# Optimization experiments

Hardware: AMD Instinct MI355X
Metric: run time of the kernel (lower is better)

Reference implementation:

```python
import jax, jax.numpy as jnp
import numpy as np

B, N, D, H = 4, 2048, 768, 12
HD = D // H
SCALE = HD ** -0.5


def setup_inputs() -> dict:
    key = jax.random.key(0)
    k1, k2, k3 = jax.random.split(key, 3)
    x = jax.random.normal(k1, (B, N, D), dtype=jnp.float32)
    w_qkv = jax.random.normal(k2, (D, 3 * D), dtype=jnp.float32) * (D ** -0.5)
    w_proj = jax.random.normal(k3, (D, D), dtype=jnp.float32) * (D ** -0.5)
    b_proj = jnp.zeros((D,), dtype=jnp.float32)
    return {"x": x, "w_qkv": w_qkv, "w_proj": w_proj, "b_proj": b_proj}


def reference(x, w_qkv, w_proj, b_proj):
    b, n, d = x.shape
    qkv = x @ w_qkv                      # [b, n, 3d]
    q, k, v = jnp.split(qkv, 3, axis=-1)
    # [b, n, d] -> [b, h, n, hd]
    split_heads = lambda t: t.reshape(b, n, H, HD).transpose(0, 2, 1, 3)
    q, k, v = split_heads(q), split_heads(k), split_heads(v)
    dots = jnp.einsum('bhqd,bhkd->bhqk', q, k) * SCALE   # [b, h, n, n]
    attn = jax.nn.softmax(dots, axis=-1)
    q_attn = attn[:, :, 0, :]            # attention row of query token 0: [b, h, n]
    # dropout p=0 (eval) -> identity
    out = jnp.einsum('bhqk,bhkd->bhqd', attn, v)          # [b, h, n, hd]
    out = out.transpose(0, 2, 1, 3).reshape(b, n, d)      # [b, n, d]
    return out @ w_proj + b_proj, q_attn
```

## Files before the change

### kernel.cpp

```cpp
#include <hip/hip_runtime.h>


typedef unsigned short u16;
typedef __attribute__((ext_vector_type(8))) short bf8;
typedef __attribute__((ext_vector_type(4))) short bf4;
typedef __attribute__((ext_vector_type(4))) int i4;
typedef __attribute__((ext_vector_type(4))) float f4;

#define MFMA16(a, b, c) __builtin_amdgcn_mfma_f32_16x16x32_bf16((a), (b), (c), 0, 0, 0)

#if __has_builtin(__builtin_amdgcn_exp2f)
#define EXP2(x) __builtin_amdgcn_exp2f(x)
#else
#define EXP2(x) __expf((x) * 0.6931471805599453f)
#endif

__device__ __forceinline__ float b2f(u16 h) {
  union { unsigned u; float f; } v; v.u = ((unsigned)h) << 16; return v.f;
}
__device__ __forceinline__ u16 f2b(float f) {
  union { float f; unsigned u; } v; v.f = f;
  unsigned r = v.u + 0x7fffu + ((v.u >> 16) & 1u);
  return (u16)(r >> 16);
}
__device__ __forceinline__ unsigned pack2(float a, float b) {
#if __has_builtin(__builtin_amdgcn_perm)
  return __builtin_amdgcn_perm(__builtin_bit_cast(unsigned, b),
                               __builtin_bit_cast(unsigned, a), 0x07060302u);
#else
  return (__builtin_bit_cast(unsigned, b) & 0xFFFF0000u) |
         (__builtin_bit_cast(unsigned, a) >> 16);
#endif
}
__device__ __forceinline__ void gload16(const u16* g, u16* l) {
  __builtin_amdgcn_global_load_lds(
      (const __attribute__((address_space(1))) void*)g,
      (__attribute__((address_space(3))) void*)l, 16, 0, 0);
}
__device__ __forceinline__ int detect_f32(const u16* x) {
  unsigned v = x[2 * (threadIdx.x & 63)];
  unsigned e = (v >> 7) & 0xFF;
  return __ballot(e >= 0x8E) != 0ull;
}

__global__ __launch_bounds__(256) void prep(
    const void* __restrict__ x, u16* __restrict__ xbf,
    const void* __restrict__ wqkv, u16* __restrict__ wqkvT,
    const void* __restrict__ wproj, u16* __restrict__ wprojT) {
  const int z = blockIdx.z;
  if (z == 2) {
    const int f32 = detect_f32((const u16*)x);
    const int lin = blockIdx.y * 72 + blockIdx.x;
    if (f32) {
      const float2* in = (const float2*)x;
      unsigned* out = (unsigned*)xbf;
      for (int i = lin * 256 + threadIdx.x; i < 3145728; i += 442368) {
        float2 v = in[i];
        out[i] = (unsigned)f2b(v.x) | ((unsigned)f2b(v.y) << 16);
      }
    } else {
      const unsigned* in = (const unsigned*)x;
      unsigned* out = (unsigned*)xbf;
      for (int i = lin * 256 + threadIdx.x; i < 3145728; i += 442368)
        out[i] = in[i];
    }
    return;
  }
  if (z == 1 && blockIdx.x >= 24) return;
  const void* in = z ? wproj : wqkv;
  u16* out = z ? wprojT : wqkvT;
  const int R = 768, C = z ? 768 : 2304;
  __shared__ u16 tile[32][33];
  const int f32 = detect_f32((const u16*)x);
  const int bx = blockIdx.x * 32, by = blockIdx.y * 32;
  const int tx = threadIdx.x & 31, ty = threadIdx.x >> 5;
#pragma unroll
  for (int i = 0; i < 4; i++) {
    size_t idx = (size_t)(by + ty + i * 8) * C + bx + tx;
    tile[ty + i * 8][tx] = f32 ? f2b(((const float*)in)[idx]) : ((const u16*)in)[idx];
  }
  __syncthreads();
#pragma unroll
  for (int i = 0; i < 4; i++)
    out[(size_t)(bx + ty + i * 8) * R + by + tx] = tile[tx][ty + i * 8];
}

__global__ __launch_bounds__(512, 2) void gemm_qkv8(
    const u16* __restrict__ A, const u16* __restrict__ Bt,
    u16* __restrict__ Cq, u16* __restrict__ Vt) {
  __shared__ alignas(16) u16 L[2][34816];
  const int t = threadIdx.x;
  const int lane = t & 63, wave = t >> 6;
  const int wr = wave >> 1, wc = wave & 1;
  const int quad = lane >> 4, l16 = lane & 15;
  const int bm = blockIdx.y * 256, bn = blockIdx.x * 288;
  const int dcol = ((lane & 3) ^ ((lane >> 3) & 3)) * 8;
  const int swzU = (quad ^ ((l16 >> 1) & 3)) * 8;
  const int drow = lane >> 2;
  f4 acc[4][9] = {};

#define STAGE_ALL(kt, buf)                                                   \
  for (int c = wave; c < 68; c += 8) {                                       \
    const int isB = c >= 32;                                                 \
    const int cb = isB ? c - 32 : c;                                         \
    const int kq_ = isB ? (cb >= 18 ? 1 : 0) : (cb >> 4);                    \
    const int r16 = isB ? (cb - kq_ * 18) : (cb & 15);                       \
    const u16* src = (isB ? Bt : A) +                                        \
        (size_t)((isB ? bn : bm) + r16 * 16 + drow) * 768 +                  \
        (kt) * 64 + kq_ * 32 + dcol;                                         \
    u16* dst = &L[buf][(isB ? 16384 + kq_ * 9216 : kq_ * 8192) + r16 * 512]; \
    gload16(src, dst);                                                       \
  }

  STAGE_ALL(0, 0);
  asm volatile("s_waitcnt vmcnt(0)" ::: "memory");
  __builtin_amdgcn_sched_barrier(0);
  __builtin_amdgcn_s_barrier();
  __builtin_amdgcn_sched_barrier(0);

  for (int j = 0; j < 12; j++) {
    const int buf = j & 1;
    if (j + 1 < 12) STAGE_ALL(j + 1, buf ^ 1);
    const u16* Lb = &L[buf][0];
    bf8 af[4][2];
#pragma unroll
    for (int m = 0; m < 4; m++)
#pragma unroll
      for (int kq = 0; kq < 2; kq++)
        af[m][kq] = *(const bf8*)&Lb[kq * 8192 +
                                     (wr * 64 + m * 16 + l16) * 32 + swzU];
#pragma unroll
    for (int p = 0; p < 3; p++) {
      bf8 bfr[3][2];
#pragma unroll
      for (int nn = 0; nn < 3; nn++)
#pragma unroll
        for (int kq = 0; kq < 2; kq++)
          bfr[nn][kq] = *(const bf8*)&Lb[16384 + kq * 9216 +
              (wc * 144 + (p * 3 + nn) * 16 + l16) * 32 + swzU];
      __builtin_amdgcn_s_setprio(1);
#pragma unroll
      for (int nn = 0; nn < 3; nn++)
#pragma unroll
        for (int m = 0; m < 4; m++) {
          acc[m][p * 3 + nn] = MFMA16(af[m][0], bfr[nn][0], acc[m][p * 3 + nn]);
          acc[m][p * 3 + nn] = MFMA16(af[m][1], bfr[nn][1], acc[m][p * 3 + nn]);
        }
      __builtin_amdgcn_s_setprio(0);
    }
    if (j + 1 < 12) {
      asm volatile("s_waitcnt vmcnt(0)" ::: "memory");
      __builtin_amdgcn_sched_barrier(0);
      __builtin_amdgcn_s_barrier();
      __builtin_amdgcn_sched_barrier(0);
    }
  }
#undef STAGE_ALL

  const int b_ = bm >> 11;
#pragma unroll
  for (int m = 0; m < 4; m++) {
    const int row0 = bm + wr * 64 + m * 16 + quad * 4;
    const int n0 = row0 & 2047;
    const int n2 = (n0 & ~31) | (((n0 >> 2) & 3) << 3) | (((n0 >> 4) & 1) << 2);
#pragma unroll
    for (int ni = 0; ni < 9; ni++) {
      const int col = bn + wc * 144 + ni * 16 + l16;
      if (col >= 1536) {
        const int colv = col - 1536, h = colv >> 6, d = colv & 63;
        bf4 pk = {(short)f2b(acc[m][ni][0]), (short)f2b(acc[m][ni][1]),
                  (short)f2b(acc[m][ni][2]), (short)f2b(acc[m][ni][3])};
        *(bf4*)&Vt[(size_t)((b_ * 12 + h) * 64 + d) * 2048 + n2] = pk;
      } else {
#pragma unroll
        for (int r = 0; r < 4; r++)
          Cq[(size_t)(row0 + r) * 2304 + col] = f2b(acc[m][ni][r]);
      }
    }
  }
}

template <int BIAS, int QATTN>
__global__ __launch_bounds__(256, 4) void gemm_bt(
    const u16* __restrict__ A, const u16* __restrict__ Bt,
    const void* __restrict__ bias, void* __restrict__ C,
    int M, int Ncols, int K, const u16* __restrict__ xdet,
    u16* __restrict__ Vt, const float* __restrict__ qe,
    const float* __restrict__ lout) {
  if (QATTN && blockIdx.x == 6) {
    const int f32o = detect_f32(xdet);
    const int base = blockIdx.y * 1536;
    for (int j = threadIdx.x; j < 1536; j += 256) {
      int idx = base + j;
      float v = qe[idx] * (1.f / lout[idx >> 11]);
      size_t oidx = (size_t)6291456 + idx;
      if (f32o) ((float*)C)[oidx] = v; else ((u16*)C)[oidx] = f2b(v);
    }
    return;
  }
  __shared__ alignas(16) u16 Al[2][128 * 32];
  __shared__ alignas(16) u16 Bl[2][128 * 32];
  const int t = threadIdx.x;
  const int lane = t & 63, wave = t >> 6;
  const int wr = wave >> 1, wc = wave & 1;
  const int quad = lane >> 4, l16 = lane & 15;
  const int bm = blockIdx.y * 128, bn = blockIdx.x * 128;
  const int f32o = BIAS ? detect_f32(xdet) : 0;
  const int grow = lane >> 2, gcol = (lane & 3) * 8;
  const int chunk0 = wave * 2, chunk1 = wave * 2 + 1;
  const int arow0 = chunk0 * 16 + grow, arow1 = chunk1 * 16 + grow;
  f4 acc[4][4] = {};
  gload16(A + (size_t)(bm + arow0) * K + gcol, &Al[0][chunk0 * 512]);
  gload16(Bt + (size_t)(bn + arow0) * K + gcol, &Bl[0][chunk0 * 512]);
  gload16(A + (size_t)(bm + arow1) * K + gcol, &Al[0][chunk1 * 512]);
  gload16(Bt + (size_t)(bn + arow1) * K + gcol, &Bl[0][chunk1 * 512]);
  const int NIT = K >> 5;
  for (int i = 0; i < NIT; i++) {
    const int cur = i & 1, nxt = cur ^ 1;
    __syncthreads();
    if (i + 1 < NIT) {
      int k0 = (i + 1) << 5;
      gload16(A + (size_t)(bm + arow0) * K + k0 + gcol, &Al[nxt][chunk0 * 512]);
      gload16(Bt + (size_t)(bn + arow0) * K + k0 + gcol, &Bl[nxt][chunk0 * 512]);
      gload16(A + (size_t)(bm + arow1) * K + k0 + gcol, &Al[nxt][chunk1 * 512]);
      gload16(Bt + (size_t)(bn + arow1) * K + k0 + gcol, &Bl[nxt][chunk1 * 512]);
    }
    bf8 af[4], bfr[4];
#pragma unroll
    for (int mt = 0; mt < 4; mt++)
      af[mt] = *(const bf8*)&Al[cur][(wr * 64 + mt * 16 + l16) * 32 + quad * 8];
#pragma unroll
    for (int nt = 0; nt < 4; nt++)
      bfr[nt] = *(const bf8*)&Bl[cur][(wc * 64 + nt * 16 + l16) * 32 + quad * 8];
#pragma unroll
    for (int mt = 0; mt < 4; mt++)
#pragma unroll
      for (int nt = 0; nt < 4; nt++)
        acc[mt][nt] = MFMA16(af[mt], bfr[nt], acc[mt][nt]);
  }
  if (Vt != nullptr && bn >= 1536) {
    const int b = bm >> 11;
#pragma unroll
    for (int mt = 0; mt < 4; mt++) {
      int n0 = (bm & 2047) + wr * 64 + mt * 16 + quad * 4;
      int n2 = (n0 & ~31) | (((n0 >> 2) & 3) << 3) | (((n0 >> 4) & 1) << 2);
#pragma unroll
      for (int nt = 0; nt < 4; nt++) {
        int colv = bn - 1536 + wc * 64 + nt * 16 + l16;
        int h = colv >> 6, d = colv & 63;
        bf4 pk = {(short)f2b(acc[mt][nt][0]), (short)f2b(acc[mt][nt][1]),
                  (short)f2b(acc[mt][nt][2]), (short)f2b(acc[mt][nt][3])};
        *(bf4*)&Vt[(size_t)((b * 12 + h) * 64 + d) * 2048 + n2] = pk;
      }
    }
    return;
  }
#pragma unroll
  for (int mt = 0; mt < 4; mt++) {
    int row = bm + wr * 64 + mt * 16 + quad * 4;
#pragma unroll
    for (int nt = 0; nt < 4; nt++) {
      int col = bn + wc * 64 + nt * 16 + l16;
      float bv = 0.f;
      if (BIAS)
        bv = f32o ? ((const float*)bias)[col] : b2f(((const u16*)bias)[col]);
#pragma unroll
      for (int r = 0; r < 4; r++) {
        size_t idx = (size_t)(row + r) * Ncols + col;
        float v = acc[mt][nt][r] + bv;
        if (f32o) ((float*)C)[idx] = v; else ((u16*)C)[idx] = f2b(v);
      }
    }
  }
}

__global__ __launch_bounds__(256, 3) void flash_attn(
    const u16* __restrict__ qkv, const u16* __restrict__ Vt,
    u16* __restrict__ O, float* __restrict__ qe, float* __restrict__ lout) {
  __shared__ alignas(16) u16 lds[3][8192];
  const int t = threadIdx.x, lane = t & 63, wave = t >> 6;
  const int quad = lane >> 4, l16 = lane & 15;
  const int id = blockIdx.x;
  const int bh = (id & 7) + 8 * (id >> 7);
  const int qtile = (id >> 3) & 15;
  const int b = bh / 12, h = bh - b * 12;
  const int q0 = qtile * 128 + wave * 32;
  const bool dumpP = (qe != nullptr) && (qtile == 0) && (wave == 0);
  const float SCALE2 = 0.125f * 1.44269504089f;
  const float mM0 = -16.f;
  bf8 qf[2][2];
#pragma unroll
  for (int qt = 0; qt < 2; qt++) {
    const u16* Qr = qkv + (size_t)(b * 2048 + q0 + qt * 16 + l16) * 2304 + h * 64;
    bf8 r0 = *(const bf8*)(Qr + quad * 8);
    bf8 r1 = *(const bf8*)(Qr + 32 + quad * 8);
#pragma unroll
    for (int j = 0; j < 8; j++) {
      qf[qt][0][j] = (short)f2b(b2f((u16)r0[j]) * SCALE2);
      qf[qt][1][j] = (short)f2b(b2f((u16)r1[j]) * SCALE2);
    }
  }
  bf8 ones;
#pragma unroll
  for (int j = 0; j < 8; j++) ones[j] = (short)0x3F80;
  const u16* Kb = qkv + (size_t)(b * 2048) * 2304 + 768 + h * 64;
  const u16* Vb = Vt + (size_t)((b * 12 + h) * 64) * 2048;
  const int drow = wave * 16 + (lane >> 2);
  const int dcol = ((lane & 3) ^ ((lane >> 3) & 3)) * 8;
  const int swz = (quad ^ ((l16 >> 1) & 3)) * 8;
  f4 o[2][4] = {};
  f4 lacc[2] = {};

#define STAGE(tile, buf)                                            \
  {                                                                 \
    int n1_ = (tile) * 64;                                          \
    const u16* Kt_ = Kb + (size_t)(n1_ + drow) * 2304 + dcol;       \
    const u16* Vr_ = Vb + (size_t)drow * 2048 + n1_ + dcol;         \
    u16* base_ = &lds[buf][wave * 512];                             \
    gload16(Kt_, base_);                                            \
    gload16(Kt_ + 32, base_ + 2048);                                \
    gload16(Vr_, base_ + 4096);                                     \
    gload16(Vr_ + 32, base_ + 6144);                                \
  }

  STAGE(0, 0);
  STAGE(1, 1);

  int cur = 0;
  for (int i = 0; i < 32; i++) {
    if (i < 31) {
      asm volatile("s_waitcnt vmcnt(4)" ::: "memory");
    } else {
      asm volatile("s_waitcnt vmcnt(0)" ::: "memory");
    }
    __builtin_amdgcn_s_barrier();
    if (i + 2 < 32) {
      int pre = cur + 2; if (pre >= 3) pre -= 3;
      STAGE(i + 2, pre);
    }
    const u16* K0 = &lds[cur][0];
    const u16* K1 = &lds[cur][2048];
    union { i4 i; bf8 b; } pf[2][2];
#pragma unroll
    for (int kt = 0; kt < 4; kt++) {
      bf8 kf0 = *(const bf8*)&K0[(kt * 16 + l16) * 32 + swz];
      bf8 kf1 = *(const bf8*)&K1[(kt * 16 + l16) * 32 + swz];
#pragma unroll
      for (int qt = 0; qt < 2; qt++) {
        f4 z = {mM0, mM0, mM0, mM0};
        z = MFMA16(kf0, qf[qt][0], z);
        z = MFMA16(kf1, qf[qt][1], z);
        float e0 = EXP2(z[0]);
        float e1 = EXP2(z[1]);
        float e2 = EXP2(z[2]);
        float e3 = EXP2(z[3]);
        if (qt == 0 && dumpP && l16 == 0) {
          f4 ev = {e0, e1, e2, e3};
          *(f4*)&qe[bh * 2048 + i * 64 + kt * 16 + quad * 4] = ev;
        }
        pf[qt][kt >> 1].i[(kt & 1) * 2 + 0] = (int)pack2(e0, e1);
        pf[qt][kt >> 1].i[(kt & 1) * 2 + 1] = (int)pack2(e2, e3);
      }
    }
#pragma unroll
    for (int pair = 0; pair < 2; pair++) {
      const u16* Vp = &lds[cur][4096 + pair * 2048];
      lacc[0] = MFMA16(ones, pf[0][pair].b, lacc[0]);
      lacc[1] = MFMA16(ones, pf[1][pair].b, lacc[1]);
#pragma unroll
      for (int nt = 0; nt < 4; nt++) {
        bf8 vf = *(const bf8*)&Vp[(nt * 16 + l16) * 32 + swz];
        o[0][nt] = MFMA16(vf, pf[0][pair].b, o[0][nt]);
        o[1][nt] = MFMA16(vf, pf[1][pair].b, o[1][nt]);
      }
    }
    cur = (cur == 2) ? 0 : cur + 1;
  }
#undef STAGE
#pragma unroll
  for (int qt = 0; qt < 2; qt++) {
    float l = lacc[qt][0];
    if (qt == 0 && dumpP && lane == 0) lout[bh] = l;
    float inv = 1.f / l;
    size_t row = (size_t)(b * 2048 + q0 + qt * 16 + l16) * 768 + h * 64;
#pragma unroll
    for (int nt = 0; nt < 4; nt++) {
      bf4 pk = {(short)f2b(o[qt][nt][0] * inv), (short)f2b(o[qt][nt][1] * inv),
                (short)f2b(o[qt][nt][2] * inv), (short)f2b(o[qt][nt][3] * inv)};
      *(bf4*)&O[row + nt * 16 + quad * 4] = pk;
    }
  }
}

__global__ __launch_bounds__(256) void qattn_row0(
    const u16* __restrict__ qkv, void* __restrict__ out,
    const u16* __restrict__ xdet) {
  const int bh = blockIdx.x, b = bh / 12, h = bh % 12;
  __shared__ float qs[64];
  __shared__ float sv[2048];
  __shared__ float red[8];
  const int t = threadIdx.x;
  const int f32o = detect_f32(xdet);
  if (t < 64) qs[t] = b2f(qkv[(size_t)(b * 2048) * 2304 + h * 64 + t]);
  __syncthreads();
  float lmax = -1e30f;
  for (int k = t; k < 2048; k += 256) {
    const u16* Kr = qkv + (size_t)(b * 2048 + k) * 2304 + 768 + h * 64;
    float acc = 0.f;
#pragma unroll
    for (int j = 0; j < 8; j++) {
      bf8 kv = *(const bf8*)(Kr + j * 8);
#pragma unroll
      for (int d = 0; d < 8; d++) acc += qs[j * 8 + d] * b2f((u16)kv[d]);
    }
    acc *= 0.125f;
    sv[k] = acc;
    lmax = fmaxf(lmax, acc);
  }
#pragma unroll
  for (int off = 32; off >= 1; off >>= 1) lmax = fmaxf(lmax, __shfl_xor(lmax, off, 64));
  if ((t & 63) == 0) red[t >> 6] = lmax;
  __syncthreads();
  const float bmax = fmaxf(fmaxf(red[0], red[1]), fmaxf(red[2], red[3]));
  float lsum = 0.f;
  for (int k = t; k < 2048; k += 256) {
    float e = __expf(sv[k] - bmax);
    sv[k] = e;
    lsum += e;
  }
#pragma unroll
  for (int off = 32; off >= 1; off >>= 1) lsum += __shfl_xor(lsum, off, 64);
  if ((t & 63) == 0) red[4 + (t >> 6)] = lsum;
  __syncthreads();
  const float inv = 1.f / (red[4] + red[5] + red[6] + red[7]);
  for (int k = t; k < 2048; k += 256) {
    size_t idx = (size_t)6291456 + (size_t)bh * 2048 + k;
    float v = sv[k] * inv;
    if (f32o) ((float*)out)[idx] = v; else ((u16*)out)[idx] = f2b(v);
  }
}

extern "C" void kernel_launch(void* const* d_in, const int* in_sizes, int n_in,
                              void* d_out, int out_size, void* d_ws, size_t ws_size,
                              hipStream_t stream) {
  const void* x_raw      = d_in[0];
  const void* w_qkv_raw  = d_in[1];
  const void* w_proj_raw = d_in[2];
  const void* b_proj_raw = d_in[3];
  const u16* xdet = (const u16*)x_raw;
  char* ws = (char*)d_ws;
  u16* xbf    = (u16*)(ws + 256);
  u16* wqkvT  = (u16*)(ws + 12583168);
  u16* wprojT = (u16*)(ws + 16122112);
  u16* qkv    = (u16*)(ws + 17301760);
  u16* Vt     = (u16*)(ws + 55050496);
  float* qe   = (float*)(ws + 67633408);
  float* lout = (float*)(ws + 68026624);
  u16* attn   = xbf;
  const bool fused = ws_size >= 68026816ull;

  prep<<<dim3(72, 24, 3), 256, 0, stream>>>(
      x_raw, xbf, w_qkv_raw, wqkvT, w_proj_raw, wprojT);
  gemm_qkv8<<<dim3(8, 32), 512, 0, stream>>>(xbf, wqkvT, qkv, Vt);
  flash_attn<<<dim3(768), 256, 0, stream>>>(qkv, Vt, attn,
                                            fused ? qe : nullptr,
                                            fused ? lout : nullptr);
  if (fused) {
    gemm_bt<1, 1><<<dim3(7, 64), 256, 0, stream>>>(
        attn, wprojT, b_proj_raw, d_out, 8192, 768, 768, xdet, nullptr, qe, lout);
  } else {
    gemm_bt<1, 0><<<dim3(6, 64), 256, 0, stream>>>(
        attn, wprojT, b_proj_raw, d_out, 8192, 768, 768, xdet, nullptr, nullptr, nullptr);
    qattn_row0<<<dim3(48), 256, 0, stream>>>(qkv, d_out, xdet);
  }
}
```

Before: 209.4 us.

## Software-pipeline attention loop so QK-exp of one tile overlaps PV of previous

Unrolls the 32-tile key loop into a two-stage software pipeline. The QK^T MFMA and exp2 for tile i now run alongside the PV MFMAs for tile i-1. V fragments are preloaded from LDS into registers after each QK stage, and the probability tiles ping-pong between two register sets. The aim is to hide the exp/pack latency and the dependency between QK and PV so the MFMA pipe stays busy. In exchange it adds about 32 VGPRs for V plus a second probability buffer, which may lower occupancy, and it adds an lgkmcnt(0) wait at each barrier.

```diff
diff --git a/kernel.cpp b/kernel.cpp
--- a/kernel.cpp
+++ b/kernel.cpp
@@ -6,6 +6,7 @@
 typedef __attribute__((ext_vector_type(4))) short bf4;
 typedef __attribute__((ext_vector_type(4))) int i4;
 typedef __attribute__((ext_vector_type(4))) float f4;
+typedef union { i4 iv; bf8 bv; } pfu;
 
 #define MFMA16(a, b, c) __builtin_amdgcn_mfma_f32_16x16x32_bf16((a), (b), (c), 0, 0, 0)
 
@@ -310,6 +311,9 @@
   const int swz = (quad ^ ((l16 >> 1) & 3)) * 8;
   f4 o[2][4] = {};
   f4 lacc[2] = {};
+  pfu pfA[2][2], pfB[2][2];
+  bf8 vf[8];
+  int cur = 0;
 
 #define STAGE(tile, buf)                                            \
   {                                                                 \
@@ -323,60 +327,111 @@
     gload16(Vr_ + 32, base_ + 6144);                                \
   }
 
+#define HEAD(DRAIN, DOSTAGE, i)                                          \
+  {                                                                      \
+    if (DRAIN) { asm volatile("s_waitcnt vmcnt(0) lgkmcnt(0)" ::: "memory"); } \
+    else { asm volatile("s_waitcnt vmcnt(4) lgkmcnt(0)" ::: "memory"); } \
+    __builtin_amdgcn_s_barrier();                                        \
+    if (DOSTAGE) {                                                       \
+      int pre_ = cur + 2; if (pre_ >= 3) pre_ -= 3;                      \
+      STAGE((i) + 2, pre_);                                              \
+    }                                                                    \
+  }
+
+#define QKEXP(i, PFC)                                                    \
+  {                                                                      \
+    const u16* K0_ = &lds[cur][0];                                       \
+    const u16* K1_ = &lds[cur][2048];                                    \
+    _Pragma("unroll")                                                    \
+    for (int kt = 0; kt < 4; kt++) {                                     \
+      bf8 kf0 = *(const bf8*)&K0_[(kt * 16 + l16) * 32 + swz];           \
+      bf8 kf1 = *(const bf8*)&K1_[(kt * 16 + l16) * 32 + swz];           \
+      _Pragma("unroll")                                                  \
+      for (int qt = 0; qt < 2; qt++) {                                   \
+        f4 z = {mM0, mM0, mM0, mM0};                                     \
+        z = MFMA16(kf0, qf[qt][0], z);                                   \
+        z = MFMA16(kf1, qf[qt][1], z);                                   \
+        float e0 = EXP2(z[0]);                                           \
+        float e1 = EXP2(z[1]);                                           \
+        float e2 = EXP2(z[2]);                                           \
+        float e3 = EXP2(z[3]);                                           \
+        if (qt == 0 && dumpP && l16 == 0) {                              \
+          f4 ev = {e0, e1, e2, e3};                                      \
+          *(f4*)&qe[bh * 2048 + (i) * 64 + kt * 16 + quad * 4] = ev;     \
+        }                                                                \
+        PFC[qt][kt >> 1].iv[(kt & 1) * 2 + 0] = (int)pack2(e0, e1);      \
+        PFC[qt][kt >> 1].iv[(kt & 1) * 2 + 1] = (int)pack2(e2, e3);      \
+      }                                                                  \
+    }                                                                    \
+  }
+
+#define PV(PFP)                                                          \
+  {                                                                      \
+    _Pragma("unroll")                                                    \
+    for (int pair = 0; pair < 2; pair++) {                               \
+      lacc[0] = MFMA16(ones, PFP[0][pair].bv, lacc[0]);                  \
+      lacc[1] = MFMA16(ones, PFP[1][pair].bv, lacc[1]);                  \
+      _Pragma("unroll")                                                  \
+      for (int nt = 0; nt < 4; nt++) {                                   \
+        o[0][nt] = MFMA16(vf[nt * 2 + pair], PFP[0][pair].bv, o[0][nt]); \
+        o[1][nt] = MFMA16(vf[nt * 2 + pair], PFP[1][pair].bv, o[1][nt]); \
+      }                                                                  \
+    }                                                                    \
+  }
+
+#define LOADVF                                                           \
+  {                                                                      \
+    _Pragma("unroll")                                                    \
+    for (int pair = 0; pair < 2; pair++) {                               \
+      const u16* Vp_ = &lds[cur][4096 + pair * 2048];                    \
+      _Pragma("unroll")                                                  \
+      for (int nt = 0; nt < 4; nt++)                                     \
+        vf[nt * 2 + pair] = *(const bf8*)&Vp_[(nt * 16 + l16) * 32 + swz]; \
+    }                                                                    \
+  }
+
+#define ADV cur = (cur == 2) ? 0 : cur + 1;
+
   STAGE(0, 0);
   STAGE(1, 1);
-
-  int cur = 0;
-  for (int i = 0; i < 32; i++) {
-    if (i < 31) {
-      asm volatile("s_waitcnt vmcnt(4)" ::: "memory");
-    } else {
-      asm volatile("s_waitcnt vmcnt(0)" ::: "memory");
-    }
-    __builtin_amdgcn_s_barrier();
-    if (i + 2 < 32) {
-      int pre = cur + 2; if (pre >= 3) pre -= 3;
-      STAGE(i + 2, pre);
-    }
-    const u16* K0 = &lds[cur][0];
-    const u16* K1 = &lds[cur][2048];
-    union { i4 i; bf8 b; } pf[2][2];
-#pragma unroll
-    for (int kt = 0; kt < 4; kt++) {
-      bf8 kf0 = *(const bf8*)&K0[(kt * 16 + l16) * 32 + swz];
-      bf8 kf1 = *(const bf8*)&K1[(kt * 16 + l16) * 32 + swz];
-#pragma unroll
-      for (int qt = 0; qt < 2; qt++) {
-        f4 z = {mM0, mM0, mM0, mM0};
-        z = MFMA16(kf0, qf[qt][0], z);
-        z = MFMA16(kf1, qf[qt][1], z);
-        float e0 = EXP2(z[0]);
-        float e1 = EXP2(z[1]);
-        float e2 = EXP2(z[2]);
-        float e3 = EXP2(z[3]);
-        if (qt == 0 && dumpP && l16 == 0) {
-          f4 ev = {e0, e1, e2, e3};
-          *(f4*)&qe[bh * 2048 + i * 64 + kt * 16 + quad * 4] = ev;
-        }
-        pf[qt][kt >> 1].i[(kt & 1) * 2 + 0] = (int)pack2(e0, e1);
-        pf[qt][kt >> 1].i[(kt & 1) * 2 + 1] = (int)pack2(e2, e3);
-      }
-    }
-#pragma unroll
-    for (int pair = 0; pair < 2; pair++) {
-      const u16* Vp = &lds[cur][4096 + pair * 2048];
-      lacc[0] = MFMA16(ones, pf[0][pair].b, lacc[0]);
-      lacc[1] = MFMA16(ones, pf[1][pair].b, lacc[1]);
-#pragma unroll
-      for (int nt = 0; nt < 4; nt++) {
-        bf8 vf = *(const bf8*)&Vp[(nt * 16 + l16) * 32 + swz];
-        o[0][nt] = MFMA16(vf, pf[0][pair].b, o[0][nt]);
-        o[1][nt] = MFMA16(vf, pf[1][pair].b, o[1][nt]);
-      }
-    }
-    cur = (cur == 2) ? 0 : cur + 1;
-  }
+  HEAD(0, 1, 0);
+  QKEXP(0, pfA);
+  LOADVF;
+  ADV;
+  HEAD(0, 1, 1);
+  QKEXP(1, pfB);
+  PV(pfA);
+  LOADVF;
+  ADV;
+  for (int k = 1; k <= 14; k++) {
+    HEAD(0, 1, 2 * k);
+    QKEXP(2 * k, pfA);
+    PV(pfB);
+    LOADVF;
+    ADV;
+    HEAD(0, 1, 2 * k + 1);
+    QKEXP(2 * k + 1, pfB);
+    PV(pfA);
+    LOADVF;
+    ADV;
+  }
+  HEAD(0, 0, 30);
+  QKEXP(30, pfA);
+  PV(pfB);
+  LOADVF;
+  ADV;
+  HEAD(1, 0, 31);
+  QKEXP(31, pfB);
+  PV(pfA);
+  LOADVF;
+  PV(pfB);
+#undef ADV
+#undef LOADVF
+#undef PV
+#undef QKEXP
+#undef HEAD
 #undef STAGE
+
 #pragma unroll
   for (int qt = 0; qt < 2; qt++) {
     float l = lacc[qt][0];
```

Result: slower. 273.9 us (+30.8%).

## Halve flash-attention waves per block, give each wave 64 query rows

Applied to the files above, without the earlier changes.

The flash attention block shrinks from four waves to two, and each wave now handles 64 query rows instead of 32. Each K/V fragment read from LDS is reused across four query tiles instead of two, which cuts LDS read traffic per MFMA. Each wave issues twice as many global-to-LDS staging loads, and the vmcnt wait count is raised to match. The cost is many more accumulator registers per wave, and occupancy is lower because there are fewer waves per block while LDS use per block is unchanged.

```diff
diff --git a/kernel.cpp b/kernel.cpp
--- a/kernel.cpp
+++ b/kernel.cpp
@@ -6,6 +6,7 @@
 typedef __attribute__((ext_vector_type(4))) short bf4;
 typedef __attribute__((ext_vector_type(4))) int i4;
 typedef __attribute__((ext_vector_type(4))) float f4;
+typedef union { i4 iv; bf8 bv; } pfu;
 
 #define MFMA16(a, b, c) __builtin_amdgcn_mfma_f32_16x16x32_bf16((a), (b), (c), 0, 0, 0)
 
@@ -274,7 +275,7 @@
   }
 }
 
-__global__ __launch_bounds__(256, 3) void flash_attn(
+__global__ __launch_bounds__(128, 2) void flash_attn(
     const u16* __restrict__ qkv, const u16* __restrict__ Vt,
     u16* __restrict__ O, float* __restrict__ qe, float* __restrict__ lout) {
   __shared__ alignas(16) u16 lds[3][8192];
@@ -284,13 +285,13 @@
   const int bh = (id & 7) + 8 * (id >> 7);
   const int qtile = (id >> 3) & 15;
   const int b = bh / 12, h = bh - b * 12;
-  const int q0 = qtile * 128 + wave * 32;
+  const int q0 = qtile * 128 + wave * 64;
   const bool dumpP = (qe != nullptr) && (qtile == 0) && (wave == 0);
   const float SCALE2 = 0.125f * 1.44269504089f;
   const float mM0 = -16.f;
-  bf8 qf[2][2];
-#pragma unroll
-  for (int qt = 0; qt < 2; qt++) {
+  bf8 qf[4][2];
+#pragma unroll
+  for (int qt = 0; qt < 4; qt++) {
     const u16* Qr = qkv + (size_t)(b * 2048 + q0 + qt * 16 + l16) * 2304 + h * 64;
     bf8 r0 = *(const bf8*)(Qr + quad * 8);
     bf8 r1 = *(const bf8*)(Qr + 32 + quad * 8);
@@ -305,22 +306,30 @@
   for (int j = 0; j < 8; j++) ones[j] = (short)0x3F80;
   const u16* Kb = qkv + (size_t)(b * 2048) * 2304 + 768 + h * 64;
   const u16* Vb = Vt + (size_t)((b * 12 + h) * 64) * 2048;
-  const int drow = wave * 16 + (lane >> 2);
+  const int drow0 = (wave * 2 + 0) * 16 + (lane >> 2);
+  const int drow1 = (wave * 2 + 1) * 16 + (lane >> 2);
   const int dcol = ((lane & 3) ^ ((lane >> 3) & 3)) * 8;
   const int swz = (quad ^ ((l16 >> 1) & 3)) * 8;
-  f4 o[2][4] = {};
-  f4 lacc[2] = {};
+  f4 o[4][4] = {};
+  f4 lacc[4] = {};
 
 #define STAGE(tile, buf)                                            \
   {                                                                 \
     int n1_ = (tile) * 64;                                          \
-    const u16* Kt_ = Kb + (size_t)(n1_ + drow) * 2304 + dcol;       \
-    const u16* Vr_ = Vb + (size_t)drow * 2048 + n1_ + dcol;         \
-    u16* base_ = &lds[buf][wave * 512];                             \
-    gload16(Kt_, base_);                                            \
-    gload16(Kt_ + 32, base_ + 2048);                                \
-    gload16(Vr_, base_ + 4096);                                     \
-    gload16(Vr_ + 32, base_ + 6144);                                \
+    const u16* Kt0_ = Kb + (size_t)(n1_ + drow0) * 2304 + dcol;     \
+    const u16* Vr0_ = Vb + (size_t)drow0 * 2048 + n1_ + dcol;       \
+    const u16* Kt1_ = Kb + (size_t)(n1_ + drow1) * 2304 + dcol;     \
+    const u16* Vr1_ = Vb + (size_t)drow1 * 2048 + n1_ + dcol;       \
+    u16* b0_ = &lds[buf][(wave * 2 + 0) * 512];                     \
+    u16* b1_ = &lds[buf][(wave * 2 + 1) * 512];                     \
+    gload16(Kt0_, b0_);                                             \
+    gload16(Kt0_ + 32, b0_ + 2048);                                 \
+    gload16(Vr0_, b0_ + 4096);                                      \
+    gload16(Vr0_ + 32, b0_ + 6144);                                 \
+    gload16(Kt1_, b1_);                                             \
+    gload16(Kt1_ + 32, b1_ + 2048);                                 \
+    gload16(Vr1_, b1_ + 4096);                                      \
+    gload16(Vr1_ + 32, b1_ + 6144);                                 \
   }
 
   STAGE(0, 0);
@@ -329,7 +338,7 @@
   int cur = 0;
   for (int i = 0; i < 32; i++) {
     if (i < 31) {
-      asm volatile("s_waitcnt vmcnt(4)" ::: "memory");
+      asm volatile("s_waitcnt vmcnt(8)" ::: "memory");
     } else {
       asm volatile("s_waitcnt vmcnt(0)" ::: "memory");
     }
@@ -340,13 +349,13 @@
     }
     const u16* K0 = &lds[cur][0];
     const u16* K1 = &lds[cur][2048];
-    union { i4 i; bf8 b; } pf[2][2];
+    pfu pf[4][2];
 #pragma unroll
     for (int kt = 0; kt < 4; kt++) {
       bf8 kf0 = *(const bf8*)&K0[(kt * 16 + l16) * 32 + swz];
       bf8 kf1 = *(const bf8*)&K1[(kt * 16 + l16) * 32 + swz];
 #pragma unroll
-      for (int qt = 0; qt < 2; qt++) {
+      for (int qt = 0; qt < 4; qt++) {
         f4 z = {mM0, mM0, mM0, mM0};
         z = MFMA16(kf0, qf[qt][0], z);
         z = MFMA16(kf1, qf[qt][1], z);
@@ -358,27 +367,29 @@
           f4 ev = {e0, e1, e2, e3};
           *(f4*)&qe[bh * 2048 + i * 64 + kt * 16 + quad * 4] = ev;
         }
-        pf[qt][kt >> 1].i[(kt & 1) * 2 + 0] = (int)pack2(e0, e1);
-        pf[qt][kt >> 1].i[(kt & 1) * 2 + 1] = (int)pack2(e2, e3);
+        pf[qt][kt >> 1].iv[(kt & 1) * 2 + 0] = (int)pack2(e0, e1);
+        pf[qt][kt >> 1].iv[(kt & 1) * 2 + 1] = (int)pack2(e2, e3);
       }
     }
 #pragma unroll
     for (int pair = 0; pair < 2; pair++) {
       const u16* Vp = &lds[cur][4096 + pair * 2048];
-      lacc[0] = MFMA16(ones, pf[0][pair].b, lacc[0]);
-      lacc[1] = MFMA16(ones, pf[1][pair].b, lacc[1]);
+#pragma unroll
+      for (int qt = 0; qt < 4; qt++)
+        lacc[qt] = MFMA16(ones, pf[qt][pair].bv, lacc[qt]);
 #pragma unroll
       for (int nt = 0; nt < 4; nt++) {
         bf8 vf = *(const bf8*)&Vp[(nt * 16 + l16) * 32 + swz];
-        o[0][nt] = MFMA16(vf, pf[0][pair].b, o[0][nt]);
-        o[1][nt] = MFMA16(vf, pf[1][pair].b, o[1][nt]);
+#pragma unroll
+        for (int qt = 0; qt < 4; qt++)
+          o[qt][nt] = MFMA16(vf, pf[qt][pair].bv, o[qt][nt]);
       }
     }
     cur = (cur == 2) ? 0 : cur + 1;
   }
 #undef STAGE
 #pragma unroll
-  for (int qt = 0; qt < 2; qt++) {
+  for (int qt = 0; qt < 4; qt++) {
     float l = lacc[qt][0];
     if (qt == 0 && dumpP && lane == 0) lout[bh] = l;
     float inv = 1.f / l;
@@ -462,7 +473,7 @@
   prep<<<dim3(72, 24, 3), 256, 0, stream>>>(
       x_raw, xbf, w_qkv_raw, wqkvT, w_proj_raw, wprojT);
   gemm_qkv8<<<dim3(8, 32), 512, 0, stream>>>(xbf, wqkvT, qkv, Vt);
-  flash_attn<<<dim3(768), 256, 0, stream>>>(qkv, Vt, attn,
+  flash_attn<<<dim3(768), 128, 0, stream>>>(qkv, Vt, attn,
                                             fused ? qe : nullptr,
                                             fused ? lout : nullptr);
   if (fused) {
```

Result: slower. 222.2 us (+6.1%).

## Triple-buffer QKV GEMM with K=32 stages and partial vmcnt waits

Applied to the files above, without the earlier changes.

The QKV projection GEMM moves from double buffering with 64-wide K tiles to a three-deep ring of 32-wide K tiles. Two stages are prefetched ahead, and each iteration waits only for the older stage (vmcnt(5)) rather than draining all loads. The goal is to hide global-to-LDS load latency behind MFMA work instead of stalling on a full vmcnt(0) each step. In exchange it runs twice as many iterations and barriers, with less MFMA work per barrier. Waves that have fewer chunks duplicate a load so every wave issues exactly five, which keeps the vmcnt count uniform.

```diff
diff --git a/kernel.cpp b/kernel.cpp
--- a/kernel.cpp
+++ b/kernel.cpp
@@ -88,7 +88,7 @@
 __global__ __launch_bounds__(512, 2) void gemm_qkv8(
     const u16* __restrict__ A, const u16* __restrict__ Bt,
     u16* __restrict__ Cq, u16* __restrict__ Vt) {
-  __shared__ alignas(16) u16 L[2][34816];
+  __shared__ alignas(16) u16 L[3][17408];
   const int t = threadIdx.x;
   const int lane = t & 63, wave = t >> 6;
   const int wr = wave >> 1, wc = wave & 1;
@@ -99,63 +99,56 @@
   const int drow = lane >> 2;
   f4 acc[4][9] = {};
 
-#define STAGE_ALL(kt, buf)                                                   \
-  for (int c = wave; c < 68; c += 8) {                                       \
-    const int isB = c >= 32;                                                 \
-    const int cb = isB ? c - 32 : c;                                         \
-    const int kq_ = isB ? (cb >= 18 ? 1 : 0) : (cb >> 4);                    \
-    const int r16 = isB ? (cb - kq_ * 18) : (cb & 15);                       \
-    const u16* src = (isB ? Bt : A) +                                        \
-        (size_t)((isB ? bn : bm) + r16 * 16 + drow) * 768 +                  \
-        (kt) * 64 + kq_ * 32 + dcol;                                         \
-    u16* dst = &L[buf][(isB ? 16384 + kq_ * 9216 : kq_ * 8192) + r16 * 512]; \
-    gload16(src, dst);                                                       \
-  }
-
-  STAGE_ALL(0, 0);
-  asm volatile("s_waitcnt vmcnt(0)" ::: "memory");
-  __builtin_amdgcn_sched_barrier(0);
-  __builtin_amdgcn_s_barrier();
-  __builtin_amdgcn_sched_barrier(0);
-
-  for (int j = 0; j < 12; j++) {
-    const int buf = j & 1;
-    if (j + 1 < 12) STAGE_ALL(j + 1, buf ^ 1);
-    const u16* Lb = &L[buf][0];
-    bf8 af[4][2];
+#define STAGE(kt, buf)                                                       \
+  {                                                                          \
+    _Pragma("unroll")                                                        \
+    for (int s = 0; s < 5; s++) {                                            \
+      int c = wave + s * 8;                                                  \
+      if (c >= 34) c = wave;            \
+      const int isB = c >= 16;                                               \
+      const int rb = isB ? c - 16 : c;                                       \
+      const u16* src = (isB ? Bt : A) +                                      \
+          (size_t)((isB ? bn : bm) + rb * 16 + drow) * 768 +                 \
+          (kt) * 32 + dcol;                                                  \
+      u16* dst = &L[buf][(isB ? 8192 : 0) + rb * 512];                       \
+      gload16(src, dst);                                                     \
+    }                                                                        \
+  }
+
+  STAGE(0, 0);
+  STAGE(1, 1);
+
+  int cur = 0;
+  for (int j = 0; j < 24; j++) {
+    if (j < 23) {
+      asm volatile("s_waitcnt vmcnt(5)" ::: "memory");
+    } else {
+      asm volatile("s_waitcnt vmcnt(0)" ::: "memory");
+    }
+    __builtin_amdgcn_s_barrier();
+    if (j + 2 < 24) {
+      int pre = cur + 2; if (pre >= 3) pre -= 3;
+      STAGE(j + 2, pre);
+    }
+    const u16* Lb = &L[cur][0];
+    bf8 af[4];
 #pragma unroll
     for (int m = 0; m < 4; m++)
-#pragma unroll
-      for (int kq = 0; kq < 2; kq++)
-        af[m][kq] = *(const bf8*)&Lb[kq * 8192 +
-                                     (wr * 64 + m * 16 + l16) * 32 + swzU];
-#pragma unroll
-    for (int p = 0; p < 3; p++) {
-      bf8 bfr[3][2];
-#pragma unroll
-      for (int nn = 0; nn < 3; nn++)
-#pragma unroll
-        for (int kq = 0; kq < 2; kq++)
-          bfr[nn][kq] = *(const bf8*)&Lb[16384 + kq * 9216 +
-              (wc * 144 + (p * 3 + nn) * 16 + l16) * 32 + swzU];
-      __builtin_amdgcn_s_setprio(1);
-#pragma unroll
-      for (int nn = 0; nn < 3; nn++)
-#pragma unroll
-        for (int m = 0; m < 4; m++) {
-          acc[m][p * 3 + nn] = MFMA16(af[m][0], bfr[nn][0], acc[m][p * 3 + nn]);
-          acc[m][p * 3 + nn] = MFMA16(af[m][1], bfr[nn][1], acc[m][p * 3 + nn]);
-        }
-      __builtin_amdgcn_s_setprio(0);
-    }
-    if (j + 1 < 12) {
-      asm volatile("s_waitcnt vmcnt(0)" ::: "memory");
-      __builtin_amdgcn_sched_barrier(0);
-      __builtin_amdgcn_s_barrier();
-      __builtin_amdgcn_sched_barrier(0);
-    }
-  }
-#undef STAGE_ALL
+      af[m] = *(const bf8*)&Lb[(wr * 64 + m * 16 + l16) * 32 + swzU];
+    bf8 bfr[9];
+#pragma unroll
+    for (int ni = 0; ni < 9; ni++)
+      bfr[ni] = *(const bf8*)&Lb[8192 + (wc * 144 + ni * 16 + l16) * 32 + swzU];
+    __builtin_amdgcn_s_setprio(1);
+#pragma unroll
+    for (int ni = 0; ni < 9; ni++)
+#pragma unroll
+      for (int m = 0; m < 4; m++)
+        acc[m][ni] = MFMA16(af[m], bfr[ni], acc[m][ni]);
+    __builtin_amdgcn_s_setprio(0);
+    cur = (cur == 2) ? 0 : cur + 1;
+  }
+#undef STAGE
 
   const int b_ = bm >> 11;
 #pragma unroll
```

After: 208.3 us. No clear change (-0.5%).
